# Optimization experiments

Hardware: AMD Instinct MI355X
Metric: run time of the kernel (lower is better)

Reference implementation:

```python
import jax, jax.numpy as jnp
import numpy as np

B, N, IN_DIM, OUT_DIM = 8, 2048, 256, 256
EDGE_P = 0.02   # adjacency density
MASK_P = 0.9    # fraction of valid nodes


def setup_inputs() -> dict:
    key = jax.random.key(0)
    ks = jax.random.split(key, 8)
    x = jax.random.normal(ks[0], (B, N, IN_DIM), dtype=jnp.float32)
    adj = (jax.random.uniform(ks[1], (B, N, N)) < EDGE_P).astype(jnp.float32)
    mask = (jax.random.uniform(ks[2], (B, N)) < MASK_P).astype(jnp.float32)
    # nn.Linear(in_dim, out_dim): W [out, in], b [out]
    lim1 = 1.0 / np.sqrt(IN_DIM)
    W = jax.random.uniform(ks[3], (OUT_DIM, IN_DIM), minval=-lim1, maxval=lim1, dtype=jnp.float32)
    b = jax.random.uniform(ks[4], (OUT_DIM,), minval=-lim1, maxval=lim1, dtype=jnp.float32)
    # nn.Linear(2*out_dim, 1): weight [1, 2D] split into a1 (acts on h_i), a2 (acts on h_j)
    lim2 = 1.0 / np.sqrt(2 * OUT_DIM)
    a1 = jax.random.uniform(ks[5], (OUT_DIM,), minval=-lim2, maxval=lim2, dtype=jnp.float32)
    a2 = jax.random.uniform(ks[6], (OUT_DIM,), minval=-lim2, maxval=lim2, dtype=jnp.float32)
    att_b = jax.random.uniform(ks[7], (), minval=-lim2, maxval=lim2, dtype=jnp.float32)
    return {"x": x, "adj": adj, "mask": mask, "W": W, "b": b, "a1": a1, "a2": a2, "att_b": att_b}


def reference(x, adj, mask, W, b, a1, a2, att_b):
    # h = Linear(x): [B, N, D]
    h = jnp.einsum('bni,di->bnd', x, W) + b
    # attention(cat([h_i, h_j])) == h_i @ a1 + h_j @ a2 + att_b (linear in each half)
    s1 = h @ a1  # [B, N] -> contributes along i
    s2 = h @ a2  # [B, N] -> contributes along j
    logits = s1[:, :, None] + s2[:, None, :] + att_b  # [B, N, N]
    att = jax.nn.sigmoid(logits) * adj
    att = att * mask[:, :, None] * mask[:, None, :]
    att = att / (jnp.sum(att, axis=-1, keepdims=True) + 1e-8)
    h_new = jnp.einsum('bij,bjd->bid', att, h)
    return h_new * mask[:, :, None]
```

## Files before the change

### kernel.cpp

```cpp
#include <hip/hip_runtime.h>
#include <hip/hip_bf16.h>

#define BB 8
#define NN 2048
#define DD 256
#define MM (BB * NN)

typedef __attribute__((ext_vector_type(8))) short bf16x8_t;
typedef __attribute__((ext_vector_type(4))) float f32x4_t;

__global__ __launch_bounds__(512) void gemm_hs(
    const float* __restrict__ x,
    const float* __restrict__ Wt,
    const float* __restrict__ bias,
    const float* __restrict__ a1,
    const float* __restrict__ a2,
    const float* __restrict__ mask,
    const float* __restrict__ attb_p,
    __hip_bfloat16* __restrict__ h,
    float* __restrict__ s1b,
    float* __restrict__ t2)
{
    __shared__ __hip_bfloat16 As[64][72];
    __shared__ __hip_bfloat16 Bs[256][72];
    __shared__ float s_p1[64], s_p2[64];

    const int tid  = threadIdx.x;
    const int w    = tid >> 6;
    const int lane = tid & 63;
    const int m16  = lane & 15;
    const int quad = lane >> 4;
    const int rg   = w & 3;
    const int cg   = w >> 2;
    const long rowBase = (long)blockIdx.x * 64;

    const int ar = tid >> 3;
    const int ac = (tid & 7) * 8;
    const int br = tid >> 1;
    const int bc = (tid & 1) * 32;

    f32x4_t acc[8];
#pragma unroll
    for (int c = 0; c < 8; c++) acc[c] = (f32x4_t){0.f, 0.f, 0.f, 0.f};

    float4 av[2], bv[8];
    {
        const float4* ag = (const float4*)(x + (rowBase + ar) * 256 + ac);
        av[0] = ag[0]; av[1] = ag[1];
        const float4* bg = (const float4*)(Wt + (long)br * 256 + bc);
#pragma unroll
        for (int q = 0; q < 8; q++) bv[q] = bg[q];
    }

    for (int k0 = 0; k0 < 256; k0 += 64) {
        __align__(16) __hip_bfloat16 ta[8];
        __align__(16) __hip_bfloat16 tb[32];
#pragma unroll
        for (int q = 0; q < 2; q++) {
            ta[q * 4 + 0] = __float2bfloat16(av[q].x);
            ta[q * 4 + 1] = __float2bfloat16(av[q].y);
            ta[q * 4 + 2] = __float2bfloat16(av[q].z);
            ta[q * 4 + 3] = __float2bfloat16(av[q].w);
        }
#pragma unroll
        for (int q = 0; q < 8; q++) {
            tb[q * 4 + 0] = __float2bfloat16(bv[q].x);
            tb[q * 4 + 1] = __float2bfloat16(bv[q].y);
            tb[q * 4 + 2] = __float2bfloat16(bv[q].z);
            tb[q * 4 + 3] = __float2bfloat16(bv[q].w);
        }

        __syncthreads();
        *(uint4*)&As[ar][ac] = *(uint4*)&ta[0];
#pragma unroll
        for (int q = 0; q < 4; q++)
            *(uint4*)&Bs[br][bc + q * 8] = *(uint4*)&tb[q * 8];
        __syncthreads();

        if (k0 < 192) {
            const int kn = k0 + 64;
            const float4* ag = (const float4*)(x + (rowBase + ar) * 256 + kn + ac);
            av[0] = ag[0]; av[1] = ag[1];
            const float4* bg = (const float4*)(Wt + (long)br * 256 + kn + bc);
#pragma unroll
            for (int q = 0; q < 8; q++) bv[q] = bg[q];
        }

#pragma unroll
        for (int kk = 0; kk < 64; kk += 32) {
            bf16x8_t af = *(const bf16x8_t*)&As[rg * 16 + m16][kk + quad * 8];
#pragma unroll
            for (int c = 0; c < 8; c++) {
                bf16x8_t bf = *(const bf16x8_t*)&Bs[cg * 128 + c * 16 + m16][kk + quad * 8];
                acc[c] = __builtin_amdgcn_mfma_f32_16x16x32_bf16(af, bf, acc[c], 0, 0, 0);
            }
        }
    }

    const int colBase = cg * 128;
    float p1[4] = {0.f, 0.f, 0.f, 0.f};
    float p2[4] = {0.f, 0.f, 0.f, 0.f};
    const long rw0 = rowBase + rg * 16 + quad * 4;
#pragma unroll
    for (int c = 0; c < 8; c++) {
        const int col = colBase + c * 16 + m16;
        const float bval = bias[col];
        const float va1  = a1[col];
        const float va2  = a2[col];
#pragma unroll
        for (int reg = 0; reg < 4; reg++) {
            const __hip_bfloat16 hv = __float2bfloat16(acc[c][reg] + bval);
            h[(rw0 + reg) * 256 + col] = hv;
            const float hr = __bfloat162float(hv);
            p1[reg] += hr * va1;
            p2[reg] += hr * va2;
        }
    }
#pragma unroll
    for (int off = 1; off < 16; off <<= 1) {
#pragma unroll
        for (int reg = 0; reg < 4; reg++) {
            p1[reg] += __shfl_xor(p1[reg], off);
            p2[reg] += __shfl_xor(p2[reg], off);
        }
    }
    if (cg == 1 && m16 == 0) {
#pragma unroll
        for (int reg = 0; reg < 4; reg++) {
            s_p1[rg * 16 + quad * 4 + reg] = p1[reg];
            s_p2[rg * 16 + quad * 4 + reg] = p2[reg];
        }
    }
    __syncthreads();
    if (cg == 0 && m16 == 0) {
        const float ab = attb_p[0];
#pragma unroll
        for (int reg = 0; reg < 4; reg++) {
            const int rl = rg * 16 + quad * 4 + reg;
            const long row = rowBase + rl;
            const float sp1 = p1[reg] + s_p1[rl];
            const float sp2 = p2[reg] + s_p2[rl];
            s1b[row] = sp1 + ab;
            t2[row]  = (mask[row] != 0.f) ? sp2 : -1e30f;
        }
    }
}

__global__ __launch_bounds__(256) void attn_agg(
    const float* __restrict__ adj,
    const float* __restrict__ mask,
    const __hip_bfloat16* __restrict__ h,
    const float* __restrict__ s1b,
    const float* __restrict__ t2,
    float* __restrict__ out)
{
    __shared__ float2 s_list[1024];
    __shared__ int    s_cnt;
    __shared__ float  s_red[4];
    __shared__ float  s_inv;
    __shared__ float2 s_part[128];

    const int tid = threadIdx.x;
    const int b   = blockIdx.x & 7;
    const int i   = blockIdx.x >> 3;
    const long row   = (long)b * NN + i;
    const long mbase = (long)b * NN;

    const float mask_i = mask[row];
    if (mask_i == 0.f) {
        out[row * 256 + tid] = 0.f;
        return;
    }
    if (tid == 0) s_cnt = 0;
    __syncthreads();

    const float si = s1b[row];
    const float4* arow = (const float4*)(adj + row * NN);
    const float4* trow = (const float4*)(t2 + mbase);

    float4 A0 = arow[tid], A1 = arow[256 + tid];
    float4 T0 = trow[tid], T1 = trow[256 + tid];

    float lsum = 0.f;
#pragma unroll
    for (int g = 0; g < 2; g++) {
        const int jb = g * 1024 + tid * 4;
        const float av[4] = {g ? A1.x : A0.x, g ? A1.y : A0.y, g ? A1.z : A0.z, g ? A1.w : A0.w};
        const float tv[4] = {g ? T1.x : T0.x, g ? T1.y : T0.y, g ? T1.z : T0.z, g ? T1.w : T0.w};
#pragma unroll
        for (int e = 0; e < 4; e++) {
            const float z   = si + tv[e];
            const float sig = __builtin_amdgcn_rcpf(1.f + __expf(-z));
            const float wgt = av[e] * sig;
            lsum += wgt;
            if (wgt != 0.f) {
                const int pos = atomicAdd(&s_cnt, 1);
                if (pos < 1024)
                    s_list[pos] = make_float2(__int_as_float((jb + e) << 9), wgt);
            }
        }
    }

#pragma unroll
    for (int off = 32; off; off >>= 1) lsum += __shfl_down(lsum, off);
    const int lane = tid & 63, wv = tid >> 6;
    if (lane == 0) s_red[wv] = lsum;
    __syncthreads();
    if (tid == 0)
        s_inv = 1.f / (s_red[0] + s_red[1] + s_red[2] + s_red[3] + 1e-8f);
    __syncthreads();

    const int cnt  = min(s_cnt, 1024);
    const float inv = s_inv * mask_i;
    const char* hb = (const char*)(h + mbase * 256);
    const int g  = tid >> 7;
    const int t  = tid & 127;
    const int t4 = t * 4;
    const int half = (cnt + 1) >> 1;
    int k       = g ? half : 0;
    const int end = g ? cnt : half;

    float accx = 0.f, accy = 0.f;
    for (; k + 8 <= end; k += 8) {
        float2 e[8];
#pragma unroll
        for (int q = 0; q < 8; q++) e[q] = s_list[k + q];
        unsigned u[8];
#pragma unroll
        for (int q = 0; q < 8; q++)
            u[q] = *(const unsigned*)(hb + (__float_as_int(e[q].x) + t4));
#pragma unroll
        for (int q = 0; q < 8; q++) {
            accx += e[q].y * __uint_as_float(u[q] << 16);
            accy += e[q].y * __uint_as_float(u[q] & 0xffff0000u);
        }
    }
    for (; k + 4 <= end; k += 4) {
        float2 e[4];
#pragma unroll
        for (int q = 0; q < 4; q++) e[q] = s_list[k + q];
        unsigned u[4];
#pragma unroll
        for (int q = 0; q < 4; q++)
            u[q] = *(const unsigned*)(hb + (__float_as_int(e[q].x) + t4));
#pragma unroll
        for (int q = 0; q < 4; q++) {
            accx += e[q].y * __uint_as_float(u[q] << 16);
            accy += e[q].y * __uint_as_float(u[q] & 0xffff0000u);
        }
    }
    for (; k < end; k++) {
        float2 ee = s_list[k];
        unsigned u = *(const unsigned*)(hb + (__float_as_int(ee.x) + t4));
        accx += ee.y * __uint_as_float(u << 16);
        accy += ee.y * __uint_as_float(u & 0xffff0000u);
    }

    if (g) s_part[t] = make_float2(accx, accy);
    __syncthreads();
    if (!g) {
        const float2 p = s_part[t];
        ((float2*)(out + row * 256))[t] =
            make_float2((accx + p.x) * inv, (accy + p.y) * inv);
    }
}

extern "C" void kernel_launch(void* const* d_in, const int* in_sizes, int n_in,
                              void* d_out, int out_size, void* d_ws, size_t ws_size,
                              hipStream_t stream) {
    const float* x    = (const float*)d_in[0];
    const float* adj  = (const float*)d_in[1];
    const float* mask = (const float*)d_in[2];
    const float* W    = (const float*)d_in[3];
    const float* bias = (const float*)d_in[4];
    const float* a1   = (const float*)d_in[5];
    const float* a2   = (const float*)d_in[6];
    const float* attb = (const float*)d_in[7];
    float* out = (float*)d_out;

    __hip_bfloat16* h = (__hip_bfloat16*)d_ws;
    float* s1b = (float*)((char*)d_ws + (size_t)MM * DD * 2);
    float* t2  = s1b + MM;

    gemm_hs<<<MM / 64, 512, 0, stream>>>(x, W, bias, a1, a2, mask, attb, h, s1b, t2);
    attn_agg<<<MM, 256, 0, stream>>>(adj, mask, h, s1b, t2, out);
}
```

Baseline: 238.4 us.

## Build per-wave neighbor lists with ballot compaction instead of shared atomics

Replaces the block-wide shared-memory atomic counter used to compact nonzero attention weights with per-wavefront ballot/popcount compaction into per-wave lists. Each wave then aggregates its own neighbor list over the full feature width using 8-byte loads, and the four partial results are summed through shared memory with a single barrier. This removes the atomic contention and two of the three block barriers. In exchange each wave's list is capped at 128 entries, and the gather work may be unevenly balanced across waves.

```diff
diff --git a/kernel.cpp b/kernel.cpp
--- a/kernel.cpp
+++ b/kernel.cpp
@@ -154,15 +154,13 @@
     const float* __restrict__ t2,
     float* __restrict__ out)
 {
-    __shared__ float2 s_list[1024];
-    __shared__ int    s_cnt;
+    __shared__ float2 s_list[4][128];
     __shared__ float  s_red[4];
-    __shared__ float  s_inv;
-    __shared__ float2 s_part[128];
-
-    const int tid = threadIdx.x;
-    const int b   = blockIdx.x & 7;
-    const int i   = blockIdx.x >> 3;
+    __shared__ float  s_part[4][256];
+
+    const int tid  = threadIdx.x;
+    const int b    = blockIdx.x & 7;
+    const int i    = blockIdx.x >> 3;
     const long row   = (long)b * NN + i;
     const long mbase = (long)b * NN;
 
@@ -171,20 +169,24 @@
         out[row * 256 + tid] = 0.f;
         return;
     }
-    if (tid == 0) s_cnt = 0;
-    __syncthreads();
+
+    const int w    = tid >> 6;
+    const int lane = tid & 63;
 
     const float si = s1b[row];
     const float4* arow = (const float4*)(adj + row * NN);
     const float4* trow = (const float4*)(t2 + mbase);
 
-    float4 A0 = arow[tid], A1 = arow[256 + tid];
-    float4 T0 = trow[tid], T1 = trow[256 + tid];
-
+    const int q0 = w * 128 + lane;
+    float4 A0 = arow[q0], A1 = arow[q0 + 64];
+    float4 T0 = trow[q0], T1 = trow[q0 + 64];
+
+    const unsigned long long lt = (1ull << lane) - 1ull;
     float lsum = 0.f;
+    int   cnt  = 0;
 #pragma unroll
     for (int g = 0; g < 2; g++) {
-        const int jb = g * 1024 + tid * 4;
+        const int jb = w * 512 + g * 256 + lane * 4;
         const float av[4] = {g ? A1.x : A0.x, g ? A1.y : A0.y, g ? A1.z : A0.z, g ? A1.w : A0.w};
         const float tv[4] = {g ? T1.x : T0.x, g ? T1.y : T0.y, g ? T1.z : T0.z, g ? T1.w : T0.w};
 #pragma unroll
@@ -193,76 +195,74 @@
             const float sig = __builtin_amdgcn_rcpf(1.f + __expf(-z));
             const float wgt = av[e] * sig;
             lsum += wgt;
+            const unsigned long long mk = __ballot(wgt != 0.f);
             if (wgt != 0.f) {
-                const int pos = atomicAdd(&s_cnt, 1);
-                if (pos < 1024)
-                    s_list[pos] = make_float2(__int_as_float((jb + e) << 9), wgt);
+                const int pos = cnt + __popcll(mk & lt);
+                if (pos < 128)
+                    s_list[w][pos] = make_float2(__int_as_float((jb + e) << 9), wgt);
             }
+            cnt += __popcll(mk);
         }
     }
 
 #pragma unroll
     for (int off = 32; off; off >>= 1) lsum += __shfl_down(lsum, off);
-    const int lane = tid & 63, wv = tid >> 6;
-    if (lane == 0) s_red[wv] = lsum;
-    __syncthreads();
-    if (tid == 0)
-        s_inv = 1.f / (s_red[0] + s_red[1] + s_red[2] + s_red[3] + 1e-8f);
-    __syncthreads();
-
-    const int cnt  = min(s_cnt, 1024);
-    const float inv = s_inv * mask_i;
+    if (lane == 0) s_red[w] = lsum;
+
     const char* hb = (const char*)(h + mbase * 256);
-    const int g  = tid >> 7;
-    const int t  = tid & 127;
-    const int t4 = t * 4;
-    const int half = (cnt + 1) >> 1;
-    int k       = g ? half : 0;
-    const int end = g ? cnt : half;
-
-    float accx = 0.f, accy = 0.f;
+    const int t8  = lane * 8;
+    const int end = min(cnt, 128);
+    float ac0 = 0.f, ac1 = 0.f, ac2 = 0.f, ac3 = 0.f;
+    int k = 0;
     for (; k + 8 <= end; k += 8) {
         float2 e[8];
 #pragma unroll
-        for (int q = 0; q < 8; q++) e[q] = s_list[k + q];
-        unsigned u[8];
+        for (int q = 0; q < 8; q++) e[q] = s_list[w][k + q];
+        uint2 u[8];
 #pragma unroll
         for (int q = 0; q < 8; q++)
-            u[q] = *(const unsigned*)(hb + (__float_as_int(e[q].x) + t4));
+            u[q] = *(const uint2*)(hb + (__float_as_int(e[q].x) + t8));
 #pragma unroll
         for (int q = 0; q < 8; q++) {
-            accx += e[q].y * __uint_as_float(u[q] << 16);
-            accy += e[q].y * __uint_as_float(u[q] & 0xffff0000u);
+            ac0 += e[q].y * __uint_as_float(u[q].x << 16);
+            ac1 += e[q].y * __uint_as_float(u[q].x & 0xffff0000u);
+            ac2 += e[q].y * __uint_as_float(u[q].y << 16);
+            ac3 += e[q].y * __uint_as_float(u[q].y & 0xffff0000u);
         }
     }
     for (; k + 4 <= end; k += 4) {
         float2 e[4];
 #pragma unroll
-        for (int q = 0; q < 4; q++) e[q] = s_list[k + q];
-        unsigned u[4];
+        for (int q = 0; q < 4; q++) e[q] = s_list[w][k + q];
+        uint2 u[4];
 #pragma unroll
         for (int q = 0; q < 4; q++)
-            u[q] = *(const unsigned*)(hb + (__float_as_int(e[q].x) + t4));
+            u[q] = *(const uint2*)(hb + (__float_as_int(e[q].x) + t8));
 #pragma unroll
         for (int q = 0; q < 4; q++) {
-            accx += e[q].y * __uint_as_float(u[q] << 16);
-            accy += e[q].y * __uint_as_float(u[q] & 0xffff0000u);
+            ac0 += e[q].y * __uint_as_float(u[q].x << 16);
+            ac1 += e[q].y * __uint_as_float(u[q].x & 0xffff0000u);
+            ac2 += e[q].y * __uint_as_float(u[q].y << 16);
+            ac3 += e[q].y * __uint_as_float(u[q].y & 0xffff0000u);
         }
     }
     for (; k < end; k++) {
-        float2 ee = s_list[k];
-        unsigned u = *(const unsigned*)(hb + (__float_as_int(ee.x) + t4));
-        accx += ee.y * __uint_as_float(u << 16);
-        accy += ee.y * __uint_as_float(u & 0xffff0000u);
-    }
-
-    if (g) s_part[t] = make_float2(accx, accy);
+        float2 ee = s_list[w][k];
+        uint2 u = *(const uint2*)(hb + (__float_as_int(ee.x) + t8));
+        ac0 += ee.y * __uint_as_float(u.x << 16);
+        ac1 += ee.y * __uint_as_float(u.x & 0xffff0000u);
+        ac2 += ee.y * __uint_as_float(u.y << 16);
+        ac3 += ee.y * __uint_as_float(u.y & 0xffff0000u);
+    }
+
+    *(float4*)&s_part[w][lane * 4] = make_float4(ac0, ac1, ac2, ac3);
+
     __syncthreads();
-    if (!g) {
-        const float2 p = s_part[t];
-        ((float2*)(out + row * 256))[t] =
-            make_float2((accx + p.x) * inv, (accy + p.y) * inv);
-    }
+
+    const float denom = s_red[0] + s_red[1] + s_red[2] + s_red[3] + 1e-8f;
+    const float inv   = mask_i / denom;
+    const float tot = s_part[0][tid] + s_part[1][tid] + s_part[2][tid] + s_part[3][tid];
+    out[row * 256 + tid] = tot * inv;
 }
 
 extern "C" void kernel_launch(void* const* d_in, const int* in_sizes, int n_in,
```

After: 240.1 us. No clear change (+0.7%).
